# Performance work log

Measured on AMD Instinct MI355X. Metric: run time of the kernel, lower is better.

Reference implementation:

```python
import jax, jax.numpy as jnp
import numpy as np

N_NODES = 100000
NEG_SLOPE = 0.2  # PyG GATConv default LeakyReLU slope


def gat_conv(x, W, att_src, att_dst, bias, edge_index, num_nodes, concat):
    """PyG-style GATConv with default add_self_loops=True.
    x: [N, Fin], W: [Fin, H*C], att_src/att_dst: [H, C], bias: [H*C] or [C].
    """
    H, C = att_src.shape
    h = (x @ W).reshape(num_nodes, H, C)              # [N, H, C]
    # append self-loops (PyG default)
    loops = jnp.arange(num_nodes, dtype=edge_index.dtype)
    src = jnp.concatenate([edge_index[0], loops])     # [E+N]
    dst = jnp.concatenate([edge_index[1], loops])
    # per-node attention logits, then per-edge score
    a_src = jnp.sum(h * att_src[None], axis=-1)       # [N, H]
    a_dst = jnp.sum(h * att_dst[None], axis=-1)       # [N, H]
    e = jax.nn.leaky_relu(a_src[src] + a_dst[dst], NEG_SLOPE)  # [E+N, H]
    # softmax over incoming edges of each destination node
    m = jax.ops.segment_max(e, dst, num_segments=num_nodes)    # [N, H]
    e = jnp.exp(e - m[dst])
    denom = jax.ops.segment_sum(e, dst, num_segments=num_nodes)
    alpha = e / denom[dst]                                      # [E+N, H]
    # scatter-aggregate weighted source features
    msg = h[src] * alpha[..., None]                             # [E+N, H, C]
    out = jax.ops.segment_sum(msg, dst, num_segments=num_nodes)  # [N, H, C]
    if concat:
        out = out.reshape(num_nodes, H * C)
    else:
        out = out.mean(axis=1)
    return out + bias


def setup_inputs() -> dict:
    key = jax.random.key(0)
    ks = jax.random.split(key, 12)
    N, E = N_NODES, 1600000
    Fin, Ch, Hh, Cout = 128, 64, 2, 64

    def glorot(k, shape):
        fan = shape[0] + shape[-1]
        return jax.random.uniform(k, shape, jnp.float32, -1.0, 1.0) * np.sqrt(6.0 / fan)

    x = jax.random.normal(ks[0], (N, Fin), jnp.float32)
    edge_index = jax.random.randint(ks[1], (2, E), 0, N, jnp.int32)
    W1 = glorot(ks[2], (Fin, Hh * Ch))
    att_src1 = glorot(ks[3], (Hh, Ch))
    att_dst1 = glorot(ks[4], (Hh, Ch))
    b1 = jnp.zeros((Hh * Ch,), jnp.float32)
    W2 = glorot(ks[5], (Hh * Ch, Cout))
    att_src2 = glorot(ks[6], (1, Cout))
    att_dst2 = glorot(ks[7], (1, Cout))
    b2 = jnp.zeros((Cout,), jnp.float32)
    return {"x": x, "edge_index": edge_index,
            "W1": W1, "att_src1": att_src1, "att_dst1": att_dst1, "b1": b1,
            "W2": W2, "att_src2": att_src2, "att_dst2": att_dst2, "b2": b2}


def reference(x, edge_index, W1, att_src1, att_dst1, b1, W2, att_src2, att_dst2, b2):
    h = gat_conv(x, W1, att_src1, att_dst1, b1, edge_index, N_NODES, concat=True)
    h = jax.nn.elu(h)
    out = gat_conv(h, W2, att_src2, att_dst2, b2, edge_index, N_NODES, concat=True)
    return out
```

## Files before the change

### kernel.cpp

```cpp
#include <hip/hip_runtime.h>
#include <hip/hip_bf16.h>
#include <cstdint>
#include <cstddef>

static constexpr int FIN = 128;
static constexpr int HC1 = 128;
static constexpr int EPB = 4096;

typedef __attribute__((ext_vector_type(8))) short short8;
typedef __attribute__((ext_vector_type(4))) float f32x4;

__device__ __forceinline__ float bf2f(unsigned int u) { return __uint_as_float(u << 16); }
__device__ __forceinline__ unsigned short f2bf(float f) {
  unsigned int u = __float_as_uint(f);
  return (unsigned short)((u + 0x7fff + ((u >> 16) & 1)) >> 16);
}
__device__ __forceinline__ float lrelu02(float x) { return x > 0.f ? x : 0.2f * x; }
__device__ __forceinline__ int rl_i(int v, int l) { return __builtin_amdgcn_readlane(v, l); }
__device__ __forceinline__ unsigned int q8b(float x, float inv) {
  float q = fminf(fmaxf(x * inv, -127.f), 127.f);
  return (unsigned int)((int)rintf(q) + 128) & 255u;
}
#define NEG_INF __int_as_float(0xff800000)

__global__ __launch_bounds__(256) void bucket_hist(const int* __restrict__ dst,
                                                   int* __restrict__ bhist, int E, int NB) {
  __shared__ int lh[512];
  int t = threadIdx.x;
  lh[t] = 0; lh[t + 256] = 0;
  __syncthreads();
  int e0 = blockIdx.x * EPB;
  #pragma unroll
  for (int i = 0; i < EPB / 256; i++) {
    int e = e0 + i * 256 + t;
    if (e < E) atomicAdd(&lh[dst[e] >> 8], 1);
  }
  __syncthreads();
  for (int x = t; x < NB; x += 256) {
    int c = lh[x];
    if (c > 0) atomicAdd(&bhist[x], c);
  }
}

__global__ __launch_bounds__(512) void scan_buckets(const int* __restrict__ bhist,
                                                    int* __restrict__ boffs, int n) {
  __shared__ int sh[512];
  int t = threadIdx.x;
  int v = (t < n) ? bhist[t] : 0;
  sh[t] = v; __syncthreads();
  for (int d = 1; d < 512; d <<= 1) {
    int w = (t >= d) ? sh[t - d] : 0;
    __syncthreads();
    sh[t] += w;
    __syncthreads();
  }
  if (t <= n) boffs[t] = sh[t] - v;
}

__global__ __launch_bounds__(256) void bucket_scatter(const int* __restrict__ src,
                                                      const int* __restrict__ dst,
                                                      const int* __restrict__ boffs,
                                                      int* __restrict__ gcur,
                                                      unsigned int* __restrict__ sorted,
                                                      int E, int NB) {
  __shared__ int lh[512];
  int t = threadIdx.x;
  lh[t] = 0; lh[t + 256] = 0;
  __syncthreads();
  int e0 = blockIdx.x * EPB;
  #pragma unroll
  for (int i = 0; i < EPB / 256; i++) {
    int e = e0 + i * 256 + t;
    if (e < E) atomicAdd(&lh[dst[e] >> 8], 1);
  }
  __syncthreads();
  for (int x = t; x < NB; x += 256) {
    int c = lh[x];
    lh[x] = (c > 0) ? (boffs[x] + atomicAdd(&gcur[x], c)) : 0;
  }
  __syncthreads();
  #pragma unroll
  for (int i = 0; i < EPB / 256; i++) {
    int e = e0 + i * 256 + t;
    if (e < E) {
      int d = dst[e];
      int pos = atomicAdd(&lh[d >> 8], 1);
      sorted[pos] = ((unsigned int)src[e] << 8) | (unsigned int)(d & 255);
    }
  }
}

__global__ __launch_bounds__(256) void bucket_place_fused(const unsigned int* __restrict__ sorted,
                                                          const int* __restrict__ boffs,
                                                          int* __restrict__ offs,
                                                          int* __restrict__ ssrc,
                                                          int N, int E) {
  __shared__ int cnt[256];
  __shared__ int pref[256];
  int b = blockIdx.x, t = threadIdx.x;
  cnt[t] = 0;
  __syncthreads();
  int beg = boffs[b], end = boffs[b + 1];
  for (int p = beg + t; p < end; p += 256)
    atomicAdd(&cnt[sorted[p] & 255u], 1);
  __syncthreads();
  int v = cnt[t];
  pref[t] = v; __syncthreads();
  for (int d = 1; d < 256; d <<= 1) {
    int w = (t >= d) ? pref[t - d] : 0;
    __syncthreads();
    pref[t] += w;
    __syncthreads();
  }
  int excl = pref[t] - v;
  int node = b * 256 + t;
  if (node < N) offs[node] = beg + excl;
  if (b == 0 && t == 0) offs[N] = E;
  cnt[t] = beg + excl;
  __syncthreads();
  for (int p = beg + t; p < end; p += 256) {
    unsigned int pk = sorted[p];
    int dl = pk & 255u;
    int r = atomicAdd(&cnt[dl], 1);
    ssrc[r] = (int)(pk >> 8);
  }
}

template <int COLS, bool AF32>
__global__ __launch_bounds__(256) void gemm_mfma(const void* __restrict__ Av,
                                                 const float* __restrict__ Wv,
                                                 const float* __restrict__ att_s,
                                                 const float* __restrict__ att_d,
                                                 unsigned char* __restrict__ Cq,
                                                 float* __restrict__ scl,
                                                 float* __restrict__ asrc,
                                                 float* __restrict__ adst,
                                                 int nrows) {
  constexpr int NT = COLS / 16;
  constexpr int H = COLS / 64;
  __shared__ unsigned short WT[COLS][136];
  __shared__ __align__(16) unsigned char pack[4][16 * COLS];

  const int tid = threadIdx.x;
  constexpr int NPC = COLS / 4;
  for (int idx = tid; idx < 128 * NPC; idx += 256) {
    int k = idx / NPC;
    int n0 = (idx - k * NPC) * 4;
    float4 wv = *(const float4*)(Wv + (size_t)k * COLS + n0);
    WT[n0 + 0][k] = f2bf(wv.x);
    WT[n0 + 1][k] = f2bf(wv.y);
    WT[n0 + 2][k] = f2bf(wv.z);
    WT[n0 + 3][k] = f2bf(wv.w);
  }

  const int w = tid >> 6, lane = tid & 63;
  const int quad = lane >> 4, cl = lane & 15;
  const int rbase = blockIdx.x * 128 + w * 32;

  float asv[NT], adv[NT];
  #pragma unroll
  for (int ct = 0; ct < NT; ct++) {
    asv[ct] = att_s[ct * 16 + cl];
    adv[ct] = att_d[ct * 16 + cl];
  }
  __syncthreads();

  f32x4 acc[2][NT];
  #pragma unroll
  for (int rt = 0; rt < 2; rt++)
    #pragma unroll
    for (int ct = 0; ct < NT; ct++) acc[rt][ct] = (f32x4){0.f, 0.f, 0.f, 0.f};

  #pragma unroll
  for (int kc = 0; kc < 4; kc++) {
    const int k0 = kc * 32 + quad * 8;
    short8 a[2];
    #pragma unroll
    for (int rt = 0; rt < 2; rt++) {
      int row = rbase + rt * 16 + cl;
      row = min(row, nrows - 1);
      if constexpr (AF32) {
        const float* ap = (const float*)Av + (size_t)row * 128 + k0;
        float4 f0 = *(const float4*)ap;
        float4 f1 = *(const float4*)(ap + 4);
        short8 t;
        t[0] = (short)f2bf(f0.x); t[1] = (short)f2bf(f0.y);
        t[2] = (short)f2bf(f0.z); t[3] = (short)f2bf(f0.w);
        t[4] = (short)f2bf(f1.x); t[5] = (short)f2bf(f1.y);
        t[6] = (short)f2bf(f1.z); t[7] = (short)f2bf(f1.w);
        a[rt] = t;
      } else {
        a[rt] = *(const short8*)((const unsigned short*)Av + (size_t)row * 128 + k0);
      }
    }
    #pragma unroll
    for (int ct = 0; ct < NT; ct++) {
      short8 b = *(const short8*)&WT[ct * 16 + cl][k0];
      #pragma unroll
      for (int rt = 0; rt < 2; rt++)
        acc[rt][ct] = __builtin_amdgcn_mfma_f32_16x16x32_bf16(a[rt], b, acc[rt][ct], 0, 0, 0);
    }
  }

  #pragma unroll
  for (int rt = 0; rt < 2; rt++) {
    #pragma unroll
    for (int r = 0; r < 4; r++) {
      int grow = rbase + rt * 16 + quad * 4 + r;
      float s0 = 0.f, s1 = 0.f, d0 = 0.f, d1 = 0.f;
      float mx = 0.f;
      #pragma unroll
      for (int ct = 0; ct < NT; ct++) {
        float av = acc[rt][ct][r];
        mx = fmaxf(mx, fabsf(av));
        if (H == 2 && ct >= NT / 2) {
          s1 = fmaf(av, asv[ct], s1);
          d1 = fmaf(av, adv[ct], d1);
        } else {
          s0 = fmaf(av, asv[ct], s0);
          d0 = fmaf(av, adv[ct], d0);
        }
      }
      #pragma unroll
      for (int dd = 8; dd >= 1; dd >>= 1) {
        mx = fmaxf(mx, __shfl_xor(mx, dd));
        s0 += __shfl_xor(s0, dd);
        d0 += __shfl_xor(d0, dd);
        if (H == 2) {
          s1 += __shfl_xor(s1, dd);
          d1 += __shfl_xor(d1, dd);
        }
      }
      float inv = mx > 0.f ? 127.f / mx : 0.f;
      if (cl == 0 && grow < nrows) {
        scl[grow] = mx * (1.f / 127.f);
        if (H == 2) {
          ((float2*)asrc)[grow] = make_float2(s0, s1);
          ((float2*)adst)[grow] = make_float2(d0, d1);
        } else {
          asrc[grow] = s0;
          adst[grow] = d0;
        }
      }
      #pragma unroll
      for (int ct = 0; ct < NT; ct++)
        pack[w][(quad * 4 + r) * COLS + ct * 16 + cl] =
            (unsigned char)q8b(acc[rt][ct][r], inv);
    }
    __syncthreads();
    if constexpr (COLS == 128) {
      #pragma unroll
      for (int i = 0; i < 2; i++) {
        int off = i * 1024 + lane * 16;
        uint4 v = *(const uint4*)&pack[w][off];
        int grow = rbase + rt * 16 + (off >> 7);
        if (grow < nrows)
          *(uint4*)(Cq + (size_t)grow * 128 + (off & 127)) = v;
      }
    } else {
      int off = lane * 16;
      uint4 v = *(const uint4*)&pack[w][off];
      int grow = rbase + rt * 16 + (off >> 6);
      if (grow < nrows)
        *(uint4*)(Cq + (size_t)grow * 64 + (off & 63)) = v;
    }
    __syncthreads();
  }
}

template <int H, bool ELU_OUT, bool F32OUT>
__global__ __launch_bounds__(256) void agg_gather(const void* __restrict__ hq,
                                                  const float* __restrict__ scl,
                                                  const float* __restrict__ asrc,
                                                  const float* __restrict__ adst,
                                                  const int* __restrict__ offs,
                                                  const int* __restrict__ ssrc,
                                                  const float* __restrict__ bias,
                                                  void* __restrict__ outv, int n) {
  __shared__ float pshare[4][64];
  __shared__ int vshare[4][64];
  const int tid = threadIdx.x;
  const int wid = tid >> 6;
  int node = (int)((blockIdx.x * (unsigned)blockDim.x + tid) >> 6);
  int lane = tid & 63;
  if (node >= n) return;
  const int hd = lane >> 5;
  const int beg = offs[node], end = offs[node + 1];
  const unsigned short* hq16 = (const unsigned short*)hq;
  const unsigned char* hqb = (const unsigned char*)hq;

  float adh, p_self, acc0, acc1;
  const float s_self = scl[node];
  if constexpr (H == 2) {
    float2 adv = ((const float2*)adst)[node];
    float2 asv = ((const float2*)asrc)[node];
    adh = hd ? adv.y : adv.x;
    p_self = __expf(lrelu02((hd ? asv.y : asv.x) + adh));
    unsigned int v = hq16[((size_t)node << 6) + lane];
    float ps = p_self * s_self;
    acc0 = ps * ((float)(v & 255u) - 128.f);
    acc1 = ps * ((float)((v >> 8) & 255u) - 128.f);
  } else {
    adh = adst[node];
    p_self = __expf(lrelu02(asrc[node] + adh));
    if (hd == 0) {
      unsigned int v = hq16[((size_t)node << 5) + lane];
      float ps = p_self * s_self;
      acc0 = ps * ((float)(v & 255u) - 128.f);
      acc1 = ps * ((float)((v >> 8) & 255u) - 128.f);
    } else {
      acc0 = 0.f; acc1 = 0.f;
    }
  }
  float dacc = 0.f;
  float SPF = 0.f;

  constexpr int CH = (H == 2) ? 32 : 64;
  const int lvoff = (lane & 31) * 2;
  for (int pos = beg; pos < end; pos += CH) {
    const int len = min(CH, end - pos);
    int li = (H == 2) ? (lane & 31) : lane;
    bool valid = li < len;
    int s_l = valid ? ssrc[pos + li] : 0;
    float scl_l = valid ? scl[s_l] : 0.f;
    float a;
    if constexpr (H == 2) a = asrc[(s_l << 1) + hd];
    else                  a = asrc[s_l];
    float e_l = lrelu02(a + adh);
    float p_l = valid ? __expf(e_l) : 0.f;
    dacc += p_l;
    p_l *= scl_l;
    SPF += p_l;
    pshare[wid][lane] = p_l;
    if constexpr (H == 1) vshare[wid][lane] = s_l << 6;

    if constexpr (H == 2) {
      const int ng = (len + 7) >> 3;
      for (int g = 0; g < ng; g++) {
        const int jb = g * 8;
        unsigned short v[8];
        #pragma unroll
        for (int k = 0; k < 8; k++) {
          int s = rl_i(s_l, jb + k);
          v[k] = hq16[((size_t)(unsigned)s << 6) + lane];
        }
        float pv[8];
        #pragma unroll
        for (int k = 0; k < 8; k++) pv[k] = pshare[wid][hd * 32 + jb + k];
        #pragma unroll
        for (int k = 0; k < 8; k++) {
          unsigned int w = v[k];
          acc0 = fmaf(pv[k], (float)(w & 255u), acc0);
          acc1 = fmaf(pv[k], (float)((w >> 8) & 255u), acc1);
        }
      }
    } else {
      const int npair = (len + 1) >> 1;
      const int ng = (npair + 7) >> 3;
      for (int g = 0; g < ng; g++) {
        const int jb = g * 16;
        unsigned short v[8];
        #pragma unroll
        for (int k = 0; k < 8; k++) {
          int voff = vshare[wid][jb + 2 * k + hd];
          v[k] = *(const unsigned short*)(hqb + (unsigned)voff + lvoff);
        }
        float pv[8];
        #pragma unroll
        for (int k = 0; k < 8; k++) pv[k] = pshare[wid][jb + 2 * k + hd];
        #pragma unroll
        for (int k = 0; k < 8; k++) {
          unsigned int w = v[k];
          acc0 = fmaf(pv[k], (float)(w & 255u), acc0);
          acc1 = fmaf(pv[k], (float)((w >> 8) & 255u), acc1);
        }
      }
    }
  }

  if constexpr (H == 2) {
    #pragma unroll
    for (int dlt = 16; dlt >= 1; dlt >>= 1) {
      dacc += __shfl_xor(dacc, dlt);
      SPF  += __shfl_xor(SPF, dlt);
    }
  } else {
    #pragma unroll
    for (int dlt = 32; dlt >= 1; dlt >>= 1) {
      dacc += __shfl_xor(dacc, dlt);
      SPF  += __shfl_xor(SPF, dlt);
    }
    acc0 += __shfl_xor(acc0, 32);
    acc1 += __shfl_xor(acc1, 32);
  }
  acc0 = fmaf(-128.f, SPF, acc0);
  acc1 = fmaf(-128.f, SPF, acc1);
  const float d = p_self + dacc;

  const float inv = 1.f / d;
  if constexpr (H == 2) {
    float2 bv = ((const float2*)bias)[lane];
    float v0 = acc0 * inv + bv.x;
    float v1 = acc1 * inv + bv.y;
    if (ELU_OUT) {
      v0 = v0 > 0.f ? v0 : (__expf(v0) - 1.f);
      v1 = v1 > 0.f ? v1 : (__expf(v1) - 1.f);
    }
    if constexpr (F32OUT) {
      ((float2*)outv)[(size_t)node * 64 + lane] = make_float2(v0, v1);
    } else {
      unsigned int pk = (unsigned int)f2bf(v0) | ((unsigned int)f2bf(v1) << 16);
      ((unsigned int*)outv)[(size_t)node * 64 + lane] = pk;
    }
  } else {
    if (hd == 0) {
      float2 bv = ((const float2*)bias)[lane];
      float v0 = acc0 * inv + bv.x;
      float v1 = acc1 * inv + bv.y;
      if (ELU_OUT) {
        v0 = v0 > 0.f ? v0 : (__expf(v0) - 1.f);
        v1 = v1 > 0.f ? v1 : (__expf(v1) - 1.f);
      }
      if constexpr (F32OUT) {
        ((float2*)outv)[(size_t)node * 32 + lane] = make_float2(v0, v1);
      } else {
        unsigned int pk = (unsigned int)f2bf(v0) | ((unsigned int)f2bf(v1) << 16);
        ((unsigned int*)outv)[(size_t)node * 32 + lane] = pk;
      }
    }
  }
}

extern "C" void kernel_launch(void* const* d_in, const int* in_sizes, int n_in,
                              void* d_out, int out_size, void* d_ws, size_t ws_size,
                              hipStream_t stream) {
  const int N = in_sizes[0] / FIN;
  const int E = in_sizes[1] / 2;

  const void*  x   = d_in[0];
  const int*   ei  = (const int*)d_in[1];
  const float* W1  = (const float*)d_in[2];
  const float* as1 = (const float*)d_in[3];
  const float* ad1 = (const float*)d_in[4];
  const float* b1  = (const float*)d_in[5];
  const float* W2  = (const float*)d_in[6];
  const float* as2 = (const float*)d_in[7];
  const float* ad2 = (const float*)d_in[8];
  const float* b2  = (const float*)d_in[9];

  const int* e_src = ei;
  const int* e_dst = ei + E;

  char* p = (char*)d_ws;
  auto carve = [&](size_t bytes) {
    char* q = p;
    p += (bytes + 255) & ~(size_t)255;
    return (void*)q;
  };
  unsigned char* h1q = (unsigned char*)carve((size_t)N * 128);
  float* scl1        = (float*)carve((size_t)N * 4);
  unsigned char* h2q = (unsigned char*)carve((size_t)N * 64);
  float* scl2        = (float*)carve((size_t)N * 4);
  unsigned short* buf2 = (unsigned short*)carve((size_t)N * HC1 * 2);
  float* asrc1 = (float*)carve((size_t)N * 2 * 4);
  float* adst1 = (float*)carve((size_t)N * 2 * 4);
  float* asrc2 = (float*)carve((size_t)N * 4);
  float* adst2 = (float*)carve((size_t)N * 4);
  int* offs    = (int*)carve((size_t)(N + 1) * 4);
  int* bhist   = (int*)carve((size_t)2 * 512 * 4);
  int* gcur    = bhist + 512;
  int* boffs   = (int*)carve(513 * 4);
  unsigned int* sorted = (unsigned int*)carve((size_t)E * 4);
  int* ssrc    = (int*)carve((size_t)E * 4);

  const int NB = (N + 255) >> 8;
  const int sgrid = (E + EPB - 1) / EPB;
  const int wgrid = (int)(((size_t)N * 64 + 255) / 256);
  const int ggrid = (N + 127) / 128;

  hipMemsetAsync(bhist, 0, (size_t)2 * 512 * 4, stream);
  bucket_hist<<<sgrid, 256, 0, stream>>>(e_dst, bhist, E, NB);
  scan_buckets<<<1, 512, 0, stream>>>(bhist, boffs, NB);
  bucket_scatter<<<sgrid, 256, 0, stream>>>(e_src, e_dst, boffs, gcur, sorted, E, NB);
  bucket_place_fused<<<NB, 256, 0, stream>>>(sorted, boffs, offs, ssrc, N, E);

  gemm_mfma<128, true><<<ggrid, 256, 0, stream>>>(x, W1, as1, ad1, h1q, scl1,
                                                  asrc1, adst1, N);
  agg_gather<2, true, false><<<wgrid, 256, 0, stream>>>(h1q, scl1, asrc1, adst1,
                                                        offs, ssrc, b1, buf2, N);

  gemm_mfma<64, false><<<ggrid, 256, 0, stream>>>(buf2, W2, as2, ad2, h2q, scl2,
                                                  asrc2, adst2, N);
  agg_gather<1, false, true><<<wgrid, 256, 0, stream>>>(h2q, scl2, asrc2, adst2,
                                                        offs, ssrc, b2, d_out, N);
}
```

Baseline: 306.3 us.

## Replace bucket sort with atomic CSR build and use fp16 dot2 in layer-1 gather

The two-level bucket sort for building the destination CSR is replaced by a per-node atomic degree histogram, a block-wise scan plus a base add, and a direct atomic scatter of source ids. In the H=2 aggregation, int8 features are turned into fp16 with the magic-number trick (OR with 0x6400) and accumulated with v_dot2 against packed fp16 attention weights. The weights are pre-scaled by 16 and the 1024 fp16 bias is removed afterwards. This aims to cut pass count in the sort and ALU work in the gather. The atomic scatter gives a nondeterministic neighbour order and makes many scattered global atomics, and the fp16 weights lose precision.

```diff
diff --git a/kernel.cpp b/kernel.cpp
--- a/kernel.cpp
+++ b/kernel.cpp
@@ -5,12 +5,12 @@
 
 static constexpr int FIN = 128;
 static constexpr int HC1 = 128;
-static constexpr int EPB = 4096;
 
 typedef __attribute__((ext_vector_type(8))) short short8;
 typedef __attribute__((ext_vector_type(4))) float f32x4;
-
-__device__ __forceinline__ float bf2f(unsigned int u) { return __uint_as_float(u << 16); }
+typedef __attribute__((ext_vector_type(2))) _Float16 f16x2;
+typedef decltype(__builtin_amdgcn_cvt_pkrtz(0.f, 0.f)) pk16x2;
+
 __device__ __forceinline__ unsigned short f2bf(float f) {
   unsigned int u = __float_as_uint(f);
   return (unsigned short)((u + 0x7fff + ((u >> 16) & 1)) >> 16);
@@ -21,25 +21,34 @@
   float q = fminf(fmaxf(x * inv, -127.f), 127.f);
   return (unsigned int)((int)rintf(q) + 128) & 255u;
 }
+__device__ __forceinline__ float fdot2u(unsigned int a, unsigned int b, float c) {
+  union { unsigned int u; f16x2 h; } ua, ub;
+  ua.u = a; ub.u = b;
+  return __builtin_amdgcn_fdot2(ua.h, ub.h, c, false);
+}
 #define NEG_INF __int_as_float(0xff800000)
 
-__global__ __launch_bounds__(256) void bucket_hist(const int* __restrict__ dst,
-                                                   int* __restrict__ bhist, int E, int NB) {
-  __shared__ int lh[512];
-  int t = threadIdx.x;
-  lh[t] = 0; lh[t + 256] = 0;
-  __syncthreads();
-  int e0 = blockIdx.x * EPB;
-  #pragma unroll
-  for (int i = 0; i < EPB / 256; i++) {
-    int e = e0 + i * 256 + t;
-    if (e < E) atomicAdd(&lh[dst[e] >> 8], 1);
-  }
-  __syncthreads();
-  for (int x = t; x < NB; x += 256) {
-    int c = lh[x];
-    if (c > 0) atomicAdd(&bhist[x], c);
-  }
+__global__ __launch_bounds__(256) void deg_hist(const int* __restrict__ dst,
+                                                int* __restrict__ cnt, int E) {
+  int i = blockIdx.x * 256 + threadIdx.x;
+  if (i < E) atomicAdd(&cnt[dst[i]], 1);
+}
+
+__global__ __launch_bounds__(256) void scan_blocks(const int* __restrict__ cnt,
+                                                   int* __restrict__ loffs,
+                                                   int* __restrict__ bsum, int N) {
+  __shared__ int sh[256];
+  int b = blockIdx.x, t = threadIdx.x, i = (b << 8) + t;
+  int v = (i < N) ? cnt[i] : 0;
+  sh[t] = v; __syncthreads();
+  for (int d = 1; d < 256; d <<= 1) {
+    int w = (t >= d) ? sh[t - d] : 0;
+    __syncthreads();
+    sh[t] += w;
+    __syncthreads();
+  }
+  if (i < N) loffs[i] = sh[t] - v;
+  if (t == 255) bsum[b] = sh[255];
 }
 
 __global__ __launch_bounds__(512) void scan_buckets(const int* __restrict__ bhist,
@@ -57,72 +66,27 @@
   if (t <= n) boffs[t] = sh[t] - v;
 }
 
-__global__ __launch_bounds__(256) void bucket_scatter(const int* __restrict__ src,
-                                                      const int* __restrict__ dst,
-                                                      const int* __restrict__ boffs,
-                                                      int* __restrict__ gcur,
-                                                      unsigned int* __restrict__ sorted,
-                                                      int E, int NB) {
-  __shared__ int lh[512];
-  int t = threadIdx.x;
-  lh[t] = 0; lh[t + 256] = 0;
-  __syncthreads();
-  int e0 = blockIdx.x * EPB;
-  #pragma unroll
-  for (int i = 0; i < EPB / 256; i++) {
-    int e = e0 + i * 256 + t;
-    if (e < E) atomicAdd(&lh[dst[e] >> 8], 1);
-  }
-  __syncthreads();
-  for (int x = t; x < NB; x += 256) {
-    int c = lh[x];
-    lh[x] = (c > 0) ? (boffs[x] + atomicAdd(&gcur[x], c)) : 0;
-  }
-  __syncthreads();
-  #pragma unroll
-  for (int i = 0; i < EPB / 256; i++) {
-    int e = e0 + i * 256 + t;
-    if (e < E) {
-      int d = dst[e];
-      int pos = atomicAdd(&lh[d >> 8], 1);
-      sorted[pos] = ((unsigned int)src[e] << 8) | (unsigned int)(d & 255);
-    }
-  }
-}
-
-__global__ __launch_bounds__(256) void bucket_place_fused(const unsigned int* __restrict__ sorted,
-                                                          const int* __restrict__ boffs,
-                                                          int* __restrict__ offs,
-                                                          int* __restrict__ ssrc,
-                                                          int N, int E) {
-  __shared__ int cnt[256];
-  __shared__ int pref[256];
-  int b = blockIdx.x, t = threadIdx.x;
-  cnt[t] = 0;
-  __syncthreads();
-  int beg = boffs[b], end = boffs[b + 1];
-  for (int p = beg + t; p < end; p += 256)
-    atomicAdd(&cnt[sorted[p] & 255u], 1);
-  __syncthreads();
-  int v = cnt[t];
-  pref[t] = v; __syncthreads();
-  for (int d = 1; d < 256; d <<= 1) {
-    int w = (t >= d) ? pref[t - d] : 0;
-    __syncthreads();
-    pref[t] += w;
-    __syncthreads();
-  }
-  int excl = pref[t] - v;
-  int node = b * 256 + t;
-  if (node < N) offs[node] = beg + excl;
-  if (b == 0 && t == 0) offs[N] = E;
-  cnt[t] = beg + excl;
-  __syncthreads();
-  for (int p = beg + t; p < end; p += 256) {
-    unsigned int pk = sorted[p];
-    int dl = pk & 255u;
-    int r = atomicAdd(&cnt[dl], 1);
-    ssrc[r] = (int)(pk >> 8);
+__global__ __launch_bounds__(256) void add_base(int* __restrict__ offs,
+                                                int* __restrict__ curs,
+                                                const int* __restrict__ bbase,
+                                                int N, int E) {
+  int i = blockIdx.x * 256 + threadIdx.x;
+  if (i < N) {
+    int o = offs[i] + bbase[i >> 8];
+    offs[i] = o;
+    curs[i] = o;
+  }
+  if (i == N) offs[N] = E;
+}
+
+__global__ __launch_bounds__(256) void scatter_edges(const int* __restrict__ src,
+                                                     const int* __restrict__ dst,
+                                                     int* __restrict__ curs,
+                                                     int* __restrict__ ssrc, int E) {
+  int i = blockIdx.x * 256 + threadIdx.x;
+  if (i < E) {
+    int pos = atomicAdd(&curs[dst[i]], 1);
+    ssrc[pos] = src[i];
   }
 }
 
@@ -279,6 +243,7 @@
                                                   void* __restrict__ outv, int n) {
   __shared__ float pshare[4][64];
   __shared__ int vshare[4][64];
+  __shared__ unsigned int ppack[4][32];
   const int tid = threadIdx.x;
   const int wid = tid >> 6;
   int node = (int)((blockIdx.x * (unsigned)blockDim.x + tid) >> 6);
@@ -297,7 +262,7 @@
     adh = hd ? adv.y : adv.x;
     p_self = __expf(lrelu02((hd ? asv.y : asv.x) + adh));
     unsigned int v = hq16[((size_t)node << 6) + lane];
-    float ps = p_self * s_self;
+    float ps = 16.f * p_self * s_self;
     acc0 = ps * ((float)(v & 255u) - 128.f);
     acc1 = ps * ((float)((v >> 8) & 255u) - 128.f);
   } else {
@@ -329,32 +294,41 @@
     float e_l = lrelu02(a + adh);
     float p_l = valid ? __expf(e_l) : 0.f;
     dacc += p_l;
-    p_l *= scl_l;
-    SPF += p_l;
-    pshare[wid][lane] = p_l;
-    if constexpr (H == 1) vshare[wid][lane] = s_l << 6;
+    float pf = p_l * scl_l;
 
     if constexpr (H == 2) {
+      pf *= 16.f;
+      float po = __shfl_xor(pf, 1);
+      float plo = (li & 1) ? po : pf;
+      float phi = (li & 1) ? pf : po;
+      union { pk16x2 h; unsigned int u; } pc;
+      pc.h = __builtin_amdgcn_cvt_pkrtz(plo, phi);
+      ppack[wid][(hd << 4) + (li >> 1)] = pc.u;
+      union { unsigned int u; f16x2 h; } oc; oc.u = pc.u;
+      SPF += (li & 1) ? (float)oc.h[1] : (float)oc.h[0];
+
       const int ng = (len + 7) >> 3;
       for (int g = 0; g < ng; g++) {
         const int jb = g * 8;
-        unsigned short v[8];
+        uint4 pp = *(const uint4*)&ppack[wid][(hd << 4) + (jb >> 1)];
+        unsigned int ppa[4] = {pp.x, pp.y, pp.z, pp.w};
         #pragma unroll
-        for (int k = 0; k < 8; k++) {
-          int s = rl_i(s_l, jb + k);
-          v[k] = hq16[((size_t)(unsigned)s << 6) + lane];
-        }
-        float pv[8];
-        #pragma unroll
-        for (int k = 0; k < 8; k++) pv[k] = pshare[wid][hd * 32 + jb + k];
-        #pragma unroll
-        for (int k = 0; k < 8; k++) {
-          unsigned int w = v[k];
-          acc0 = fmaf(pv[k], (float)(w & 255u), acc0);
-          acc1 = fmaf(pv[k], (float)((w >> 8) & 255u), acc1);
+        for (int k = 0; k < 4; k++) {
+          int s0 = rl_i(s_l, jb + 2 * k);
+          int s1 = rl_i(s_l, jb + 2 * k + 1);
+          unsigned int v0 = hq16[((size_t)(unsigned)s0 << 6) + lane];
+          unsigned int v1 = hq16[((size_t)(unsigned)s1 << 6) + lane];
+          unsigned int comb = (v1 << 16) | v0;
+          unsigned int lo = (comb & 0x00FF00FFu) | 0x64006400u;
+          unsigned int hi = ((comb >> 8) & 0x00FF00FFu) | 0x64006400u;
+          acc0 = fdot2u(ppa[k], lo, acc0);
+          acc1 = fdot2u(ppa[k], hi, acc1);
         }
       }
     } else {
+      SPF += pf;
+      pshare[wid][lane] = pf;
+      vshare[wid][lane] = s_l << 6;
       const int npair = (len + 1) >> 1;
       const int ng = (npair + 7) >> 3;
       for (int g = 0; g < ng; g++) {
@@ -384,21 +358,10 @@
       dacc += __shfl_xor(dacc, dlt);
       SPF  += __shfl_xor(SPF, dlt);
     }
-  } else {
-    #pragma unroll
-    for (int dlt = 32; dlt >= 1; dlt >>= 1) {
-      dacc += __shfl_xor(dacc, dlt);
-      SPF  += __shfl_xor(SPF, dlt);
-    }
-    acc0 += __shfl_xor(acc0, 32);
-    acc1 += __shfl_xor(acc1, 32);
-  }
-  acc0 = fmaf(-128.f, SPF, acc0);
-  acc1 = fmaf(-128.f, SPF, acc1);
-  const float d = p_self + dacc;
-
-  const float inv = 1.f / d;
-  if constexpr (H == 2) {
+    acc0 = fmaf(-1152.f, SPF, acc0);
+    acc1 = fmaf(-1152.f, SPF, acc1);
+    const float d = p_self + dacc;
+    const float inv = 0.0625f / d;
     float2 bv = ((const float2*)bias)[lane];
     float v0 = acc0 * inv + bv.x;
     float v1 = acc1 * inv + bv.y;
@@ -413,6 +376,17 @@
       ((unsigned int*)outv)[(size_t)node * 64 + lane] = pk;
     }
   } else {
+    #pragma unroll
+    for (int dlt = 32; dlt >= 1; dlt >>= 1) {
+      dacc += __shfl_xor(dacc, dlt);
+      SPF  += __shfl_xor(SPF, dlt);
+    }
+    acc0 += __shfl_xor(acc0, 32);
+    acc1 += __shfl_xor(acc1, 32);
+    acc0 = fmaf(-128.f, SPF, acc0);
+    acc1 = fmaf(-128.f, SPF, acc1);
+    const float d = p_self + dacc;
+    const float inv = 1.f / d;
     if (hd == 0) {
       float2 bv = ((const float2*)bias)[lane];
       float v0 = acc0 * inv + bv.x;
@@ -467,22 +441,22 @@
   float* asrc2 = (float*)carve((size_t)N * 4);
   float* adst2 = (float*)carve((size_t)N * 4);
   int* offs    = (int*)carve((size_t)(N + 1) * 4);
-  int* bhist   = (int*)carve((size_t)2 * 512 * 4);
-  int* gcur    = bhist + 512;
-  int* boffs   = (int*)carve(513 * 4);
-  unsigned int* sorted = (unsigned int*)carve((size_t)E * 4);
+  int* curs    = (int*)carve((size_t)N * 4);
+  int* bsum    = (int*)carve(512 * 4);
+  int* bbase   = (int*)carve(513 * 4);
   int* ssrc    = (int*)carve((size_t)E * 4);
 
   const int NB = (N + 255) >> 8;
-  const int sgrid = (E + EPB - 1) / EPB;
+  const int egrid = (E + 255) >> 8;
   const int wgrid = (int)(((size_t)N * 64 + 255) / 256);
   const int ggrid = (N + 127) / 128;
 
-  hipMemsetAsync(bhist, 0, (size_t)2 * 512 * 4, stream);
-  bucket_hist<<<sgrid, 256, 0, stream>>>(e_dst, bhist, E, NB);
-  scan_buckets<<<1, 512, 0, stream>>>(bhist, boffs, NB);
-  bucket_scatter<<<sgrid, 256, 0, stream>>>(e_src, e_dst, boffs, gcur, sorted, E, NB);
-  bucket_place_fused<<<NB, 256, 0, stream>>>(sorted, boffs, offs, ssrc, N, E);
+  hipMemsetAsync(curs, 0, (size_t)N * 4, stream);
+  deg_hist<<<egrid, 256, 0, stream>>>(e_dst, curs, E);
+  scan_blocks<<<NB, 256, 0, stream>>>(curs, offs, bsum, N);
+  scan_buckets<<<1, 512, 0, stream>>>(bsum, bbase, NB);
+  add_base<<<NB, 256, 0, stream>>>(offs, curs, bbase, N, E);
+  scatter_edges<<<egrid, 256, 0, stream>>>(e_src, e_dst, curs, ssrc, E);
 
   gemm_mfma<128, true><<<ggrid, 256, 0, stream>>>(x, W1, as1, ad1, h1q, scl1,
                                                   asrc1, adst1, N);
```

After: 446.0 us. +45.6%, slower.
